# Kernel tuning notes

Measured on AMD Instinct MI355X. Metric: run time of the kernel, lower is better.

Reference implementation:

```python
import jax, jax.numpy as jnp
import numpy as np

VOCAB = 128
EMBED = 256
HIDDEN = 1024
SEQ = 512
BATCH = 128


def setup_inputs() -> dict:
    key = jax.random.key(0)
    ks = jax.random.split(key, 16)
    bound = 1.0 / np.sqrt(HIDDEN)
    u = lambda k, shape: jax.random.uniform(k, shape, jnp.float32, -bound, bound)
    inp = {
        "x": jax.random.randint(ks[0], (SEQ, BATCH), 0, VOCAB),
        "emb": jax.random.normal(ks[1], (VOCAB, EMBED), jnp.float32),
        "W_ix": u(ks[2], (EMBED, HIDDEN)), "W_ih": u(ks[3], (HIDDEN, HIDDEN)), "b_i": u(ks[4], (HIDDEN,)),
        "W_fx": u(ks[5], (EMBED, HIDDEN)), "W_fh": u(ks[6], (HIDDEN, HIDDEN)), "b_f": u(ks[7], (HIDDEN,)) + 1.0,
        "W_gx": u(ks[8], (EMBED, HIDDEN)), "W_gh": u(ks[9], (HIDDEN, HIDDEN)), "b_g": u(ks[10], (HIDDEN,)),
        "W_ox": u(ks[11], (EMBED, HIDDEN)), "W_oh": u(ks[12], (HIDDEN, HIDDEN)), "b_o": u(ks[13], (HIDDEN,)),
        "W_cls": u(ks[14], (VOCAB, HIDDEN)),  # torch Linear weight [out, in]
        "b_cls": u(ks[15], (VOCAB,)),
    }
    return inp


def reference(x, emb, W_ix, W_ih, b_i, W_fx, W_fh, b_f,
              W_gx, W_gh, b_g, W_ox, W_oh, b_o, W_cls, b_cls):
    embeds = emb[x]  # [T, B, E]
    # Precompute all input->gate projections in one batched GEMM each.
    xi = jnp.einsum('tbe,eh->tbh', embeds, W_ix) + b_i
    xf = jnp.einsum('tbe,eh->tbh', embeds, W_fx) + b_f
    xg = jnp.einsum('tbe,eh->tbh', embeds, W_gx) + b_g
    xo = jnp.einsum('tbe,eh->tbh', embeds, W_ox) + b_o

    B = x.shape[1]
    h0 = jnp.zeros((B, HIDDEN), jnp.float32)
    c0 = jnp.zeros((B, HIDDEN), jnp.float32)

    def step(carry, gates_t):
        h, c = carry
        xi_t, xf_t, xg_t, xo_t = gates_t
        i = jax.nn.sigmoid(xi_t + h @ W_ih)
        f = jax.nn.sigmoid(xf_t + h @ W_fh)
        g = jnp.tanh(xg_t + h @ W_gh)
        o = jax.nn.sigmoid(xo_t + h @ W_oh)
        c_new = f * c + i * g
        h_new = o * jnp.tanh(c_new)
        return (h_new, c_new), h_new

    _, h_all = jax.lax.scan(step, (h0, c0), (xi, xf, xg, xo))  # [T, B, H]
    logits = jnp.einsum('tbh,vh->tbv', h_all, W_cls) + b_cls  # [T, B, V]
    return logits
```

## Files before the change

### kernel.cpp

```cpp
#include <hip/hip_runtime.h>
#include <hip/hip_bf16.h>

#define VOCAB  128
#define EMBED  256
#define HIDDEN 1024
#define SEQ    512
#define BATCH  128
#define NGCOL  4096
#define NCOL   4224

typedef short s8v __attribute__((ext_vector_type(8)));
typedef float f4  __attribute__((ext_vector_type(4)));
typedef unsigned u4v __attribute__((ext_vector_type(4)));

__device__ __forceinline__ unsigned short f2bf(float f) {
    unsigned u = __float_as_uint(f);
    u += 0x7fffu + ((u >> 16) & 1u);
    return (unsigned short)(u >> 16);
}
__device__ __forceinline__ float sigm(float x) { return 1.f / (1.f + __expf(-x)); }
__device__ __forceinline__ float tanh_(float x) {
    x = fminf(fmaxf(x, -15.f), 15.f);
    float e = __expf(2.f * x);
    return (e - 1.f) / (e + 1.f);
}

__device__ __forceinline__ void st_dword_wt(float* p, float v) {
    asm volatile("global_store_dword %0, %1, off sc0 sc1" :: "v"(p), "v"(v) : "memory");
}
__device__ __forceinline__ void st_b128_wt(unsigned short* p, u4v v) {
    asm volatile("global_store_dwordx4 %0, %1, off sc0 sc1" :: "v"(p), "v"(v) : "memory");
}
__device__ __forceinline__ void st_flag_wt(unsigned* p, unsigned v) {
    asm volatile("global_store_dword %0, %1, off sc0 sc1" :: "v"(p), "v"(v) : "memory");
}

__global__ void k_pack(const float* __restrict__ Wi, const float* __restrict__ Wf,
                       const float* __restrict__ Wg, const float* __restrict__ Wo,
                       unsigned short* __restrict__ Bp) {
    int idx = blockIdx.x * 256 + threadIdx.x;
    int k = idx >> 10, j = idx & 1023;
    int src = k * HIDDEN + j;
    size_t base = ((size_t)(j >> 2) * 128 + (k >> 3)) * 128 + ((j & 3) << 5) + (k & 7);
    Bp[base]      = f2bf(Wi[src]);
    Bp[base + 8]  = f2bf(Wf[src]);
    Bp[base + 16] = f2bf(Wg[src]);
    Bp[base + 24] = f2bf(Wo[src]);
}

__global__ void k_packc(const float* __restrict__ Wcls, unsigned short* __restrict__ Bp) {
    int idx = blockIdx.x * 256 + threadIdx.x;
    int v = idx >> 10, k = idx & 1023;
    int p = NGCOL + v;
    Bp[((size_t)(p >> 4) * 128 + (k >> 3)) * 128 + (p & 15) * 8 + (k & 7)] = f2bf(Wcls[v * HIDDEN + k]);
}

__global__ void k_proj(const float* __restrict__ emb,
                       const float* __restrict__ Wix, const float* __restrict__ Wfx,
                       const float* __restrict__ Wgx, const float* __restrict__ Wox,
                       const float* __restrict__ bi,  const float* __restrict__ bf_,
                       const float* __restrict__ bg,  const float* __restrict__ bo,
                       float* __restrict__ proj) {
    int idx = blockIdx.x * 256 + threadIdx.x;
    int j = idx & 1023;
    int g = (idx >> 10) & 3;
    int v = idx >> 12;
    const float* W  = (g == 0) ? Wix : (g == 1) ? Wfx : (g == 2) ? Wgx : Wox;
    const float* bb = (g == 0) ? bi  : (g == 1) ? bf_ : (g == 2) ? bg  : bo;
    float s = bb[j];
    const float* er = emb + v * EMBED;
    #pragma unroll 4
    for (int e = 0; e < EMBED; ++e) s = fmaf(er[e], W[e * HIDDEN + j], s);
    proj[(size_t)v * NGCOL + j * 4 + g] = s;
}

__global__ __launch_bounds__(512, 1) void k_lstm(
        const unsigned short* __restrict__ Bp, const float* __restrict__ proj,
        const int* __restrict__ x, unsigned short* __restrict__ hb,
        float* __restrict__ out, const float* __restrict__ bcls,
        unsigned* __restrict__ bar) {
    __shared__ unsigned short ldsB[65536];
    __shared__ float ldsR[4096];

    const int b = blockIdx.x;
    const int ct = b >> 1, rt = b & 1;
    const bool gateblk = (ct < 64);
    const int tid = threadIdx.x;
    const int w = tid >> 6, lane = tid & 63;
    const int rm = w >> 1, kh = w & 1;
    const int l16 = lane & 15, lhi = lane >> 4;
    const int wrow0 = rt * 64 + rm * 16;
    const int fnA = kh * 2, fnB = kh * 2 + 1;

    unsigned* goflag = bar + 256 + b * 16;

    {
        const s8v* src = (const s8v*)(Bp + (size_t)ct * 65536);
        s8v* dst = (s8v*)ldsB;
        #pragma unroll
        for (int i = 0; i < 16; ++i) dst[tid + i * 512] = src[tid + i * 512];
    }
    __syncthreads();

    const unsigned short* bb0 = ldsB + (0 * 128 + kh * 64 + lhi) * 128 + l16 * 8;
    const unsigned short* bb1 = ldsB + (1 * 128 + kh * 64 + lhi) * 128 + l16 * 8;
    const unsigned short* bb2 = ldsB + (2 * 128 + kh * 64 + lhi) * 128 + l16 * 8;
    const unsigned short* bb3 = ldsB + (3 * 128 + kh * 64 + lhi) * 128 + l16 * 8;
    float* red = ldsR + rm * 1024;

    float creg[2][4];
    #pragma unroll
    for (int c2 = 0; c2 < 2; ++c2)
        #pragma unroll
        for (int r = 0; r < 4; ++r) creg[c2][r] = 0.f;

    float bcA = 0.f, bcB = 0.f;
    int v0 = 0;
    if (!gateblk) {
        v0 = (ct - 64) * 64 + l16;
        bcA = bcls[v0 + fnA * 16];
        bcB = bcls[v0 + fnB * 16];
    }

    const int pcolA = ct * 64 + kh * 32 + l16;

    int xsr[4];
    if (gateblk) {
        #pragma unroll
        for (int r = 0; r < 4; ++r) xsr[r] = x[wrow0 + lhi * 4 + r];
    }

    for (int s = 0; s <= SEQ; ++s) {
        const unsigned short* hr = hb + (s & 1) * (BATCH * HIDDEN);
        unsigned short* hw = hb + ((s + 1) & 1) * (BATCH * HIDDEN);
        const bool work = gateblk ? (s < SEQ) : (s > 0);

        f4 c0 = {0,0,0,0}, c1 = {0,0,0,0}, c2 = {0,0,0,0}, c3 = {0,0,0,0};
        float pfA[4], pfB[4];
        s8v av[16];

        if (work) {
            const unsigned short* aptr = hr + (wrow0 + l16) * HIDDEN + kh * 512 + lhi * 8;

#define A_LOAD(I)                                                                 \
            asm volatile("global_load_dwordx4 %0, %1, off sc0 sc1"                \
                         : "=&v"(av[I]) : "v"(aptr + (I) * 32));
            A_LOAD(0) A_LOAD(1) A_LOAD(2) A_LOAD(3) A_LOAD(4) A_LOAD(5)

#define K_ITER(I, W)                                                              \
            {                                                                     \
                s8v bv0 = *(const s8v*)(bb0 + (I) * 512);                         \
                s8v bv1 = *(const s8v*)(bb1 + (I) * 512);                         \
                s8v bv2 = *(const s8v*)(bb2 + (I) * 512);                         \
                s8v bv3 = *(const s8v*)(bb3 + (I) * 512);                         \
                if ((I) + 6 < 16) { A_LOAD((I) + 6) }                             \
                asm volatile("s_waitcnt vmcnt(" #W ")" ::: "memory");             \
                __builtin_amdgcn_sched_barrier(0);                                \
                c0 = __builtin_amdgcn_mfma_f32_16x16x32_bf16(av[I], bv0, c0, 0, 0, 0); \
                c1 = __builtin_amdgcn_mfma_f32_16x16x32_bf16(av[I], bv1, c1, 0, 0, 0); \
                c2 = __builtin_amdgcn_mfma_f32_16x16x32_bf16(av[I], bv2, c2, 0, 0, 0); \
                c3 = __builtin_amdgcn_mfma_f32_16x16x32_bf16(av[I], bv3, c3, 0, 0, 0); \
            }
#define PF_LOAD(R)                                                                \
            { const float* pr = proj + (size_t)xsr[R] * NGCOL + pcolA;            \
              asm volatile("global_load_dword %0, %2, off\n\t"                    \
                           "global_load_dword %1, %3, off"                        \
                           : "=&v"(pfA[R]), "=&v"(pfB[R])                         \
                           : "v"(pr), "v"(pr + 16)); }

            if (gateblk) {
                K_ITER(0, 6) K_ITER(1, 6) K_ITER(2, 6) K_ITER(3, 6)
                K_ITER(4, 6) K_ITER(5, 6)
                PF_LOAD(0) PF_LOAD(1) PF_LOAD(2) PF_LOAD(3)
                K_ITER(6, 14) K_ITER(7, 14) K_ITER(8, 14) K_ITER(9, 14)
                K_ITER(10, 13) K_ITER(11, 12) K_ITER(12, 3) K_ITER(13, 2)
                K_ITER(14, 1) K_ITER(15, 0)
            } else {
                K_ITER(0, 6) K_ITER(1, 6) K_ITER(2, 6) K_ITER(3, 6)
                K_ITER(4, 6) K_ITER(5, 6) K_ITER(6, 6) K_ITER(7, 6)
                K_ITER(8, 6) K_ITER(9, 6) K_ITER(10, 5) K_ITER(11, 4)
                K_ITER(12, 3) K_ITER(13, 2) K_ITER(14, 1) K_ITER(15, 0)
            }

            if (gateblk && s + 1 < SEQ) {
                const int* xp = x + (s + 1) * BATCH + wrow0 + lhi * 4;
#define X_LOAD(R)                                                                 \
                asm volatile("global_load_dword %0, %1, off"                      \
                             : "=&v"(xsr[R]) : "v"(xp + (R)));
                X_LOAD(0) X_LOAD(1) X_LOAD(2) X_LOAD(3)
            }
            if (kh == 0) {
                #pragma unroll
                for (int r = 0; r < 4; ++r) {
                    red[(2 * 4 + r) * 64 + lane] = c2[r];
                    red[(3 * 4 + r) * 64 + lane] = c3[r];
                }
            } else {
                #pragma unroll
                for (int r = 0; r < 4; ++r) {
                    red[(0 * 4 + r) * 64 + lane] = c0[r];
                    red[(1 * 4 + r) * 64 + lane] = c1[r];
                }
            }
        }
        __syncthreads();
        if (work) {
            f4 accA, accB;
            if (kh == 0) {
                #pragma unroll
                for (int r = 0; r < 4; ++r) {
                    accA[r] = c0[r] + red[(0 * 4 + r) * 64 + lane];
                    accB[r] = c1[r] + red[(1 * 4 + r) * 64 + lane];
                }
            } else {
                #pragma unroll
                for (int r = 0; r < 4; ++r) {
                    accA[r] = c2[r] + red[(2 * 4 + r) * 64 + lane];
                    accB[r] = c3[r] + red[(3 * 4 + r) * 64 + lane];
                }
            }
            if (gateblk) {
                const bool isg = (lane & 3) == 2;
                const int qb = lane & ~3;
                #pragma unroll
                for (int r = 0; r < 4; ++r) {
                    int row = wrow0 + lhi * 4 + r;
                    float preA = accA[r] + pfA[r];
                    float preB = accB[r] + pfB[r];
                    float xA = isg ? preA + preA : preA;
                    float xB = isg ? preB + preB : preB;
                    float sA = sigm(xA), sB = sigm(xB);
                    float actA = isg ? sA + sA - 1.f : sA;
                    float actB = isg ? sB + sB - 1.f : sB;
                    float iA = __shfl(actA, qb),     iB = __shfl(actB, qb);
                    float fA = __shfl(actA, qb | 1), fB = __shfl(actB, qb | 1);
                    float gA = __shfl(actA, qb | 2), gB = __shfl(actB, qb | 2);
                    float oA = __shfl(actA, qb | 3), oB = __shfl(actB, qb | 3);
                    float cnA = fA * creg[0][r] + iA * gA; creg[0][r] = cnA;
                    float cnB = fB * creg[1][r] + iB * gB; creg[1][r] = cnB;
                    float hvA = oA * tanh_(cnA);
                    float hvB = oB * tanh_(cnB);
                    float hnA = __shfl(hvA, lane ^ 4);
                    float hnB = __shfl(hvB, lane ^ 4);
                    unsigned packA = (unsigned)f2bf(hvA) | ((unsigned)f2bf(hnA) << 16);
                    unsigned packB = (unsigned)f2bf(hvB) | ((unsigned)f2bf(hnB) << 16);
                    unsigned packA2 = __shfl(packA, (lane & ~15) | 8);
                    unsigned packB2 = __shfl(packB, (lane & ~15) | 8);
                    if (l16 == 0) {
                        u4v pk = {packA, packA2, packB, packB2};
                        st_b128_wt(hw + row * HIDDEN + ct * 16 + kh * 8, pk);
                    }
                }
            } else {
                float* ob = out + (size_t)(s - 1) * (BATCH * VOCAB);
#define DO_LOGIT(ACC, FN, BC)                                                     \
                _Pragma("unroll")                                                 \
                for (int r = 0; r < 4; ++r) {                                     \
                    int row = wrow0 + lhi * 4 + r;                                \
                    st_dword_wt(ob + row * VOCAB + v0 + (FN) * 16, ACC[r] + BC);  \
                }
                DO_LOGIT(accA, fnA, bcA)
                DO_LOGIT(accB, fnB, bcB)
            }
        }
        if (s < SEQ) {
            asm volatile("s_waitcnt vmcnt(0)" ::: "memory");
            __builtin_amdgcn_sched_barrier(0);
            __syncthreads();
            const unsigned ep = (unsigned)(s + 1);
            if (w == 0) {
                unsigned bcast = 0;
                if (lane == 0) {
                    unsigned old = __hip_atomic_fetch_add(bar + (rt * 8 + ct / 11) * 16, 1u,
                                        __ATOMIC_RELAXED, __HIP_MEMORY_SCOPE_AGENT);
                    if (old % 11u == 10u) {
                        unsigned mold = __hip_atomic_fetch_add(bar + (rt * 8 + 6) * 16, 1u,
                                            __ATOMIC_RELAXED, __HIP_MEMORY_SCOPE_AGENT);
                        if (mold == 6u * ep - 1u) bcast = 1u;
                    }
                }
                bcast = __shfl(bcast, 0);
                if (bcast) {
                    st_flag_wt(bar + 256 + (2 * lane + rt) * 16, ep);
                    if (lane < 2)
                        st_flag_wt(bar + 256 + (2 * (64 + lane) + rt) * 16, ep);
                }
                if (lane == 0) {
                    while (__hip_atomic_load(goflag, __ATOMIC_RELAXED,
                                             __HIP_MEMORY_SCOPE_AGENT) < ep)
                        __builtin_amdgcn_s_sleep(1);
                }
            }
            __syncthreads();
        }
    }
}

extern "C" void kernel_launch(void* const* d_in, const int* in_sizes, int n_in,
                              void* d_out, int out_size, void* d_ws, size_t ws_size,
                              hipStream_t stream) {
    (void)in_sizes; (void)n_in; (void)out_size; (void)ws_size;
    const int*   x    = (const int*)d_in[0];
    const float* emb  = (const float*)d_in[1];
    const float* Wix  = (const float*)d_in[2];
    const float* Wih  = (const float*)d_in[3];
    const float* bi   = (const float*)d_in[4];
    const float* Wfx  = (const float*)d_in[5];
    const float* Wfh  = (const float*)d_in[6];
    const float* bf   = (const float*)d_in[7];
    const float* Wgx  = (const float*)d_in[8];
    const float* Wgh  = (const float*)d_in[9];
    const float* bg   = (const float*)d_in[10];
    const float* Wox  = (const float*)d_in[11];
    const float* Woh  = (const float*)d_in[12];
    const float* bo   = (const float*)d_in[13];
    const float* Wcls = (const float*)d_in[14];
    const float* bcls = (const float*)d_in[15];
    float* out = (float*)d_out;

    char* ws = (char*)d_ws;
    unsigned*       bar  = (unsigned*)ws;
    unsigned short* hb   = (unsigned short*)(ws + 16384);
    float*          proj = (float*)(ws + 540672);
    unsigned short* Bp   = (unsigned short*)(ws + 2637824);

    (void)hipMemsetAsync(ws, 0, 278528, stream);

    k_pack <<<4096, 256, 0, stream>>>(Wih, Wfh, Wgh, Woh, Bp);
    k_packc<<<512,  256, 0, stream>>>(Wcls, Bp);
    k_proj <<<2048, 256, 0, stream>>>(emb, Wix, Wfx, Wgx, Wox, bi, bf, bg, bo, proj);
    k_lstm <<<132,  512, 0, stream>>>(Bp, proj, x, hb, out, bcls, bar);
}
```

Measured before the change: 3.967 ms.

## Replace global grid barrier with per-block dataflow flags and triple-buffered h

Removes the hierarchical atomic grid barrier that ran after every timestep. Each block now waits only on the per-block flags of the 32 producer blocks covering its K-half of h, and signals its own readiness after writing h. The h ping-pong buffer becomes three buffers. A 'done' flag tracks when readers have finished step s-1, so the buffer about to be overwritten is not clobbered. This lets blocks run ahead of each other and cuts barrier latency, at the cost of more flag polling traffic and subtle memory-ordering risk with relaxed atomics.

```diff
diff --git a/kernel.cpp b/kernel.cpp
--- a/kernel.cpp
+++ b/kernel.cpp
@@ -92,7 +92,10 @@
     const int wrow0 = rt * 64 + rm * 16;
     const int fnA = kh * 2, fnB = kh * 2 + 1;
 
-    unsigned* goflag = bar + 256 + b * 16;
+    unsigned* hflag = bar + 512;
+    unsigned* done  = bar + 1024;
+    unsigned* myhflag = hflag + rt * 64 + ct;
+    unsigned* mydone  = done + rt * 128 + ct;
 
     {
         const s8v* src = (const s8v*)(Bp + (size_t)ct * 65536);
@@ -131,8 +134,8 @@
     }
 
     for (int s = 0; s <= SEQ; ++s) {
-        const unsigned short* hr = hb + (s & 1) * (BATCH * HIDDEN);
-        unsigned short* hw = hb + ((s + 1) & 1) * (BATCH * HIDDEN);
+        const unsigned short* hr = hb + (s % 3) * (BATCH * HIDDEN);
+        unsigned short* hw = hb + ((s + 1) % 3) * (BATCH * HIDDEN);
         const bool work = gateblk ? (s < SEQ) : (s > 0);
 
         f4 c0 = {0,0,0,0}, c1 = {0,0,0,0}, c2 = {0,0,0,0}, c3 = {0,0,0,0};
@@ -140,6 +143,20 @@
         s8v av[16];
 
         if (work) {
+            if (s > 0) {
+                const unsigned* hf = hflag + rt * 64 + kh * 32;
+                const unsigned tgt = (unsigned)s;
+                for (;;) {
+                    unsigned v = tgt;
+                    if (lane < 32)
+                        v = __hip_atomic_load(hf + lane, __ATOMIC_RELAXED,
+                                              __HIP_MEMORY_SCOPE_AGENT);
+                    if (__ballot(v >= tgt) == ~0ull) break;
+                    __builtin_amdgcn_s_sleep(1);
+                }
+                __builtin_amdgcn_sched_barrier(0);
+            }
+
             const unsigned short* aptr = hr + (wrow0 + l16) * HIDDEN + kh * 512 + lhi * 8;
 
 #define A_LOAD(I)                                                                 \
@@ -204,6 +221,7 @@
             }
         }
         __syncthreads();
+        if (tid == 0) st_flag_wt(mydone, (unsigned)(s + 1));
         if (work) {
             f4 accA, accB;
             if (kh == 0) {
@@ -220,6 +238,21 @@
                 }
             }
             if (gateblk) {
+                if (s >= 2) {
+                    const unsigned* dn = done + rt * 128;
+                    const unsigned tgt = (unsigned)(s - 1);
+                    for (;;) {
+                        unsigned v1 = __hip_atomic_load(dn + lane, __ATOMIC_RELAXED,
+                                                        __HIP_MEMORY_SCOPE_AGENT);
+                        unsigned v2 = tgt;
+                        if (lane < 2)
+                            v2 = __hip_atomic_load(dn + 64 + lane, __ATOMIC_RELAXED,
+                                                   __HIP_MEMORY_SCOPE_AGENT);
+                        if (__ballot(v1 >= tgt && v2 >= tgt) == ~0ull) break;
+                        __builtin_amdgcn_s_sleep(1);
+                    }
+                    __builtin_amdgcn_sched_barrier(0);
+                }
                 const bool isg = (lane & 3) == 2;
                 const int qb = lane & ~3;
                 #pragma unroll
@@ -263,35 +296,11 @@
                 DO_LOGIT(accB, fnB, bcB)
             }
         }
-        if (s < SEQ) {
+        if (gateblk && s < SEQ) {
             asm volatile("s_waitcnt vmcnt(0)" ::: "memory");
             __builtin_amdgcn_sched_barrier(0);
             __syncthreads();
-            const unsigned ep = (unsigned)(s + 1);
-            if (w == 0) {
-                unsigned bcast = 0;
-                if (lane == 0) {
-                    unsigned old = __hip_atomic_fetch_add(bar + (rt * 8 + ct / 11) * 16, 1u,
-                                        __ATOMIC_RELAXED, __HIP_MEMORY_SCOPE_AGENT);
-                    if (old % 11u == 10u) {
-                        unsigned mold = __hip_atomic_fetch_add(bar + (rt * 8 + 6) * 16, 1u,
-                                            __ATOMIC_RELAXED, __HIP_MEMORY_SCOPE_AGENT);
-                        if (mold == 6u * ep - 1u) bcast = 1u;
-                    }
-                }
-                bcast = __shfl(bcast, 0);
-                if (bcast) {
-                    st_flag_wt(bar + 256 + (2 * lane + rt) * 16, ep);
-                    if (lane < 2)
-                        st_flag_wt(bar + 256 + (2 * (64 + lane) + rt) * 16, ep);
-                }
-                if (lane == 0) {
-                    while (__hip_atomic_load(goflag, __ATOMIC_RELAXED,
-                                             __HIP_MEMORY_SCOPE_AGENT) < ep)
-                        __builtin_amdgcn_s_sleep(1);
-                }
-            }
-            __syncthreads();
+            if (tid == 0) st_flag_wt(myhflag, (unsigned)(s + 1));
         }
     }
 }
@@ -321,8 +330,8 @@
     char* ws = (char*)d_ws;
     unsigned*       bar  = (unsigned*)ws;
     unsigned short* hb   = (unsigned short*)(ws + 16384);
-    float*          proj = (float*)(ws + 540672);
-    unsigned short* Bp   = (unsigned short*)(ws + 2637824);
+    float*          proj = (float*)(ws + 802816);
+    unsigned short* Bp   = (unsigned short*)(ws + 2899968);
 
     (void)hipMemsetAsync(ws, 0, 278528, stream);
 
```

After: 5.029 ms. 1.27x slower.
